# Optimization experiments

Hardware: AMD Instinct MI355X
Metric: run time of the kernel (lower is better)

The kernel has to match this reference:

```python
import jax, jax.numpy as jnp
import numpy as np

WINDOW_SIZE = (8, 8, 8)
DIM = 256
NUM_HEADS = 8
NUM_WINDOWS = 16
BATCH = 128  # num_windows * B
N = int(np.prod(WINDOW_SIZE))  # 512


def _make_rpb_buffers(ws):
    space = len(ws)
    coords = [np.arange(-(w - 1), w, dtype=np.float32) for w in ws]
    rpb = np.stack(np.meshgrid(*coords, indexing='ij'))  # (space, 2w-1, ...)
    for i in range(space):
        rpb[i] = rpb[i] / (ws[i] - 1)
    rpb = np.moveaxis(rpb, 0, -1)[None]  # (1, ..., space)
    rpb = 8.0 * rpb
    rpb = np.sign(rpb) * np.log2(np.abs(rpb) + 1.0) / np.log2(8.0)
    grid = np.stack(np.meshgrid(*[np.arange(w) for w in ws], indexing='ij'))
    g = grid.reshape(space, -1).astype(np.int64)
    dists = g[:, :, None] - g[:, None, :]  # (space, N, N)
    for i in range(space):
        center = max(int(np.prod([2 * w - 1 for w in ws[i + 1:]])), 1)
        dists[i] = (dists[i] + ws[i] - 1) * center
    rpb_idx = dists.sum(0)  # (N, N)
    return rpb.astype(np.float32), rpb_idx.astype(np.int32)


def setup_inputs() -> dict:
    key = jax.random.key(0)
    ks = jax.random.split(key, 8)
    rpb_np, rpb_idx_np = _make_rpb_buffers(WINDOW_SIZE)
    s = 0.02
    return {
        'x': jax.random.normal(ks[0], (BATCH, N, DIM), dtype=jnp.float32),
        'mask': jnp.zeros((NUM_WINDOWS, N, N), dtype=jnp.float32),
        'qkv_w': jax.random.normal(ks[1], (3 * DIM, DIM), dtype=jnp.float32) * s,
        'proj_w': jax.random.normal(ks[2], (DIM, DIM), dtype=jnp.float32) * s,
        'proj_b': jnp.zeros((DIM,), dtype=jnp.float32),
        'cpb_w1': jax.random.normal(ks[3], (512, 3), dtype=jnp.float32) * s,
        'cpb_b1': jnp.zeros((512,), dtype=jnp.float32),
        'cpb_w2': jax.random.normal(ks[4], (NUM_HEADS, 512), dtype=jnp.float32) * s,
        'rpb': jnp.asarray(rpb_np),
        'rpb_idx': jnp.asarray(rpb_idx_np),
    }


def reference(x, mask, qkv_w, proj_w, proj_b, cpb_w1, cpb_b1, cpb_w2, rpb, rpb_idx):
    b, n, c = x.shape
    h = cpb_w2.shape[0]
    hd = c // h
    # qkv projection (no bias), split into q,k,v of shape (b, h, n, hd)
    qkv = jnp.einsum('bnc,oc->bno', x, qkv_w).reshape(b, n, 3, h, hd)
    qkv = jnp.transpose(qkv, (2, 0, 3, 1, 4))
    q, k, v = qkv[0], qkv[1], qkv[2]
    # continuous relative-position bias: MLP over log-spaced coords, gather, sigmoid
    hidden = jax.nn.relu(jnp.einsum('...d,od->...o', rpb, cpb_w1) + cpb_b1)
    table = jnp.einsum('...o,ho->...h', hidden, cpb_w2).reshape(-1, h)  # (prod(2w-1), h)
    rpb_bias = table[rpb_idx.reshape(-1)].reshape(n, n, h)
    rpb_bias = 16.0 * jax.nn.sigmoid(rpb_bias)
    rpb_bias = jnp.transpose(rpb_bias, (2, 0, 1))[None]  # (1, h, n, n)
    # mask (nw, n, n) -> (b, 1, n, n) via repeat along batch
    nw = mask.shape[0]
    m = jnp.tile(mask[:, None, :, :], (b // nw, 1, 1, 1))
    bias = m + rpb_bias  # (b, h, n, n)
    # scaled dot-product attention
    scale = 1.0 / jnp.sqrt(jnp.float32(hd))
    scores = jnp.einsum('bhqd,bhkd->bhqk', q, k) * scale + bias
    attn = jax.nn.softmax(scores, axis=-1)
    out = jnp.einsum('bhqk,bhkd->bhqd', attn, v)
    out = jnp.transpose(out, (0, 2, 1, 3)).reshape(b, n, c)
    out = jnp.einsum('bnc,oc->bno', out, proj_w) + proj_b
    return out
```

## Files before the change

### kernel.cpp

```cpp
#include <hip/hip_runtime.h>
#include <hip/hip_bf16.h>


using u16 = unsigned short;
using u32 = unsigned int;
typedef short bf16x4 __attribute__((ext_vector_type(4)));
typedef short bf16x8 __attribute__((ext_vector_type(8)));
typedef float f32x4 __attribute__((ext_vector_type(4)));

#define QSL 0.25503471f
#define LOG2E 1.44269504f
#define CMB_SHIFT 11.65f

static __device__ __forceinline__ u32 cvt_pk_bf16(float lo, float hi) {
  u32 r;
  asm("v_cvt_pk_bf16_f32 %0, %1, %2" : "=v"(r) : "v"(lo), "v"(hi));
  return r;
}

__global__ __launch_bounds__(512) void cpb_kernel(
    const float* __restrict__ rpb, const float* __restrict__ w1,
    const float* __restrict__ b1, const float* __restrict__ w2,
    float* __restrict__ table16) {
  __shared__ float hid[512];
  const int p = blockIdx.x;
  const int t = threadIdx.x;
  const float r0 = rpb[p * 3 + 0], r1 = rpb[p * 3 + 1], r2 = rpb[p * 3 + 2];
  float hv = fmaf(r0, w1[t * 3 + 0],
             fmaf(r1, w1[t * 3 + 1],
             fmaf(r2, w1[t * 3 + 2], b1[t])));
  hid[t] = fmaxf(hv, 0.0f);
  __syncthreads();
  const int h = t >> 6, lane = t & 63;
  float s = 0.0f;
#pragma unroll
  for (int u = 0; u < 8; ++u)
    s = fmaf(hid[lane + u * 64], w2[h * 512 + lane + u * 64], s);
#pragma unroll
  for (int off = 32; off > 0; off >>= 1) s += __shfl_down(s, off);
  if (lane == 0) table16[p * 8 + h] = 23.08312065f / (1.0f + __expf(-s));
}

__global__ __launch_bounds__(256) void cmb_kernel(
    const int* __restrict__ rpb_idx, const float* __restrict__ table16,
    const float* __restrict__ mask, u16* __restrict__ cmb) {
  const int ij0 = (blockIdx.x * 256 + threadIdx.x) * 4;
  const int w = blockIdx.y;
  const float4 m4 = *reinterpret_cast<const float4*>(mask + (size_t)w * 262144 + ij0);
  const int4 i4 = *reinterpret_cast<const int4*>(rpb_idx + ij0);
  float ta[8], tb[8], tc[8], td[8];
  *reinterpret_cast<float4*>(&ta[0]) = *reinterpret_cast<const float4*>(table16 + i4.x * 8);
  *reinterpret_cast<float4*>(&ta[4]) = *reinterpret_cast<const float4*>(table16 + i4.x * 8 + 4);
  *reinterpret_cast<float4*>(&tb[0]) = *reinterpret_cast<const float4*>(table16 + i4.y * 8);
  *reinterpret_cast<float4*>(&tb[4]) = *reinterpret_cast<const float4*>(table16 + i4.y * 8 + 4);
  *reinterpret_cast<float4*>(&tc[0]) = *reinterpret_cast<const float4*>(table16 + i4.z * 8);
  *reinterpret_cast<float4*>(&tc[4]) = *reinterpret_cast<const float4*>(table16 + i4.z * 8 + 4);
  *reinterpret_cast<float4*>(&td[0]) = *reinterpret_cast<const float4*>(table16 + i4.w * 8);
  *reinterpret_cast<float4*>(&td[4]) = *reinterpret_cast<const float4*>(table16 + i4.w * 8 + 4);
  const float b0 = m4.x * LOG2E - CMB_SHIFT;
  const float b1 = m4.y * LOG2E - CMB_SHIFT;
  const float b2 = m4.z * LOG2E - CMB_SHIFT;
  const float b3 = m4.w * LOG2E - CMB_SHIFT;
  u16* outp = cmb + (size_t)w * 8 * 262144 + ij0;
#pragma unroll
  for (int h = 0; h < 8; ++h) {
    uint2 o;
    o.x = cvt_pk_bf16(ta[h] + b0, tb[h] + b1);
    o.y = cvt_pk_bf16(tc[h] + b2, td[h] + b3);
    *reinterpret_cast<uint2*>(outp + (size_t)h * 262144) = o;
  }
}

__global__ __launch_bounds__(256, 2) void qkv_mfma(
    const float* __restrict__ x, const float* __restrict__ w,
    u16* __restrict__ qbuf, u16* __restrict__ kbuf, u16* __restrict__ vbuf) {
  __shared__ u16 As[128 * 64];
  __shared__ u16 Bs0[128 * 64];
  __shared__ u16 Bs1[128 * 64];
  const int tid = threadIdx.x;
  const int flat = blockIdx.x;
  const int wrk = (flat & 7) * 192 + (flat >> 3);
  const int bm = wrk / 3;
  const int bnp = wrk - bm * 3;
  const int m0 = bm * 128, n0 = bnp * 256;
  const float scl = (bnp == 0) ? QSL : 1.0f;
  u16* dst = bnp == 0 ? qbuf : (bnp == 1 ? kbuf : vbuf);
  const int lane = tid & 63, wid = tid >> 6;
  const int wm = wid >> 1, wn = wid & 1;
  const int lq = lane & 15, g = lane >> 4;
  const f32x4 fz = {0.f, 0.f, 0.f, 0.f};
  f32x4 acc0[4][4], acc1[4][4];
#pragma unroll
  for (int i = 0; i < 4; ++i)
#pragma unroll
    for (int j = 0; j < 4; ++j) { acc0[i][j] = fz; acc1[i][j] = fz; }

  const int r0 = tid >> 3;
  const int ch = tid & 7;
  const int sx = (ch ^ (r0 & 7)) << 3;

  for (int k0 = 0; k0 < 256; k0 += 64) {
    __syncthreads();
#pragma unroll
    for (int rr = 0; rr < 4; ++rr) {
      const int r = r0 + rr * 32;
      const float* ax = x + (size_t)(m0 + r) * 256 + k0 + ch * 8;
      const float4 a0 = *reinterpret_cast<const float4*>(ax);
      const float4 a1 = *reinterpret_cast<const float4*>(ax + 4);
      const float* bx0 = w + (size_t)(n0 + r) * 256 + k0 + ch * 8;
      const float* bx1 = w + (size_t)(n0 + 128 + r) * 256 + k0 + ch * 8;
      const float4 b00 = *reinterpret_cast<const float4*>(bx0);
      const float4 b01 = *reinterpret_cast<const float4*>(bx0 + 4);
      const float4 b10 = *reinterpret_cast<const float4*>(bx1);
      const float4 b11 = *reinterpret_cast<const float4*>(bx1 + 4);
      uint4 pk;
      pk.x = cvt_pk_bf16(a0.x, a0.y); pk.y = cvt_pk_bf16(a0.z, a0.w);
      pk.z = cvt_pk_bf16(a1.x, a1.y); pk.w = cvt_pk_bf16(a1.z, a1.w);
      *reinterpret_cast<uint4*>(&As[r * 64 + sx]) = pk;
      pk.x = cvt_pk_bf16(b00.x * scl, b00.y * scl);
      pk.y = cvt_pk_bf16(b00.z * scl, b00.w * scl);
      pk.z = cvt_pk_bf16(b01.x * scl, b01.y * scl);
      pk.w = cvt_pk_bf16(b01.z * scl, b01.w * scl);
      *reinterpret_cast<uint4*>(&Bs0[r * 64 + sx]) = pk;
      pk.x = cvt_pk_bf16(b10.x * scl, b10.y * scl);
      pk.y = cvt_pk_bf16(b10.z * scl, b10.w * scl);
      pk.z = cvt_pk_bf16(b11.x * scl, b11.y * scl);
      pk.w = cvt_pk_bf16(b11.z * scl, b11.w * scl);
      *reinterpret_cast<uint4*>(&Bs1[r * 64 + sx]) = pk;
    }
    __syncthreads();
#pragma unroll
    for (int ks = 0; ks < 2; ++ks) {
      bf16x8 xf[4];
#pragma unroll
      for (int mt = 0; mt < 4; ++mt) {
        const int row = wm * 64 + mt * 16 + lq;
        xf[mt] = *reinterpret_cast<const bf16x8*>(
            &As[row * 64 + (((ks * 4 + g) ^ (row & 7)) << 3)]);
      }
#pragma unroll
      for (int nt = 0; nt < 4; ++nt) {
        const int row = wn * 64 + nt * 16 + lq;
        const int off = row * 64 + (((ks * 4 + g) ^ (row & 7)) << 3);
        const bf16x8 wf0 = *reinterpret_cast<const bf16x8*>(&Bs0[off]);
        const bf16x8 wf1 = *reinterpret_cast<const bf16x8*>(&Bs1[off]);
#pragma unroll
        for (int mt = 0; mt < 4; ++mt) {
          acc0[mt][nt] = __builtin_amdgcn_mfma_f32_16x16x32_bf16(
              wf0, xf[mt], acc0[mt][nt], 0, 0, 0);
          acc1[mt][nt] = __builtin_amdgcn_mfma_f32_16x16x32_bf16(
              wf1, xf[mt], acc1[mt][nt], 0, 0, 0);
        }
      }
    }
  }
#pragma unroll
  for (int mt = 0; mt < 4; ++mt) {
    const int m = m0 + wm * 64 + mt * 16 + lq;
    const int b = m >> 9, ii = m & 511;
#pragma unroll
    for (int nt = 0; nt < 4; ++nt) {
      const int nn = wn * 64 + nt * 16 + 4 * g;
      {
        const int n = n0 + nn;
        const int h = (n & 255) >> 5;
        const int d = n & 31;
        const size_t off = ((size_t)(b * 8 + h) * 512 + ii) * 32 + d;
        uint2 o2;
        o2.x = cvt_pk_bf16(acc0[mt][nt][0], acc0[mt][nt][1]);
        o2.y = cvt_pk_bf16(acc0[mt][nt][2], acc0[mt][nt][3]);
        *reinterpret_cast<uint2*>(dst + off) = o2;
      }
      {
        const int n = n0 + 128 + nn;
        const int h = (n & 255) >> 5;
        const int d = n & 31;
        const size_t off = ((size_t)(b * 8 + h) * 512 + ii) * 32 + d;
        uint2 o2;
        o2.x = cvt_pk_bf16(acc1[mt][nt][0], acc1[mt][nt][1]);
        o2.y = cvt_pk_bf16(acc1[mt][nt][2], acc1[mt][nt][3]);
        *reinterpret_cast<uint2*>(dst + off) = o2;
      }
    }
  }
}

__global__ __launch_bounds__(256, 2) void attn_mfma(
    u16* qbuf,
    const u16* __restrict__ kbuf, const u16* __restrict__ vbuf,
    const u16* __restrict__ cmb) {
  __shared__ u16 Klds[512 * 32];
  __shared__ u16 Vtlds[32 * 512];
  const int t = threadIdx.x;
  const int qc = blockIdx.x, h = blockIdx.y;
  const int bz = blockIdx.z;
  const int b = ((bz & 15) << 3) | (bz >> 4);
  const size_t bh = (size_t)b * 8 + h;
  const u16* kb = kbuf + bh * 16384;
  const u16* vb = vbuf + bh * 16384;

#pragma unroll
  for (int c = 0; c < 8; ++c) {
    const int cid = t + c * 256;
    const int key = cid >> 2, ch = cid & 3;
    const uint4 kd = *reinterpret_cast<const uint4*>(kb + cid * 8);
    const int idx = key * 32 + ((ch * 8) ^ (((key >> 1) & 3) << 3));
    *reinterpret_cast<uint4*>(&Klds[idx]) = kd;
  }
#pragma unroll
  for (int r = 0; r < 2; ++r) {
    const int n = t + r * 256;
    const uint4 v0 = *reinterpret_cast<const uint4*>(vb + n * 32);
    const uint4 v1 = *reinterpret_cast<const uint4*>(vb + n * 32 + 8);
    const uint4 v2 = *reinterpret_cast<const uint4*>(vb + n * 32 + 16);
    const uint4 v3 = *reinterpret_cast<const uint4*>(vb + n * 32 + 24);
    const u32 wv16[16] = {v0.x, v0.y, v0.z, v0.w, v1.x, v1.y, v1.z, v1.w,
                          v2.x, v2.y, v2.z, v2.w, v3.x, v3.y, v3.z, v3.w};
#pragma unroll
    for (int u = 0; u < 16; ++u) {
      const int d0 = 2 * u, d1 = 2 * u + 1;
      Vtlds[d0 * 512 + (n ^ ((d0 & 7) << 3))] = (u16)(wv16[u] & 0xffffu);
      Vtlds[d1 * 512 + (n ^ ((d1 & 7) << 3))] = (u16)(wv16[u] >> 16);
    }
  }
  __syncthreads();

  const int lane = t & 63;
  const int lq = lane & 15, g = lane >> 4;
  const int wv = t >> 6;
  const int q0 = qc * 256 + wv * 64;

  bf16x8 Qf[4];
  u16* qrowbase = qbuf + bh * 16384;
#pragma unroll
  for (int qt = 0; qt < 4; ++qt)
    Qf[qt] = *reinterpret_cast<const bf16x8*>(qrowbase + (q0 + qt * 16 + lq) * 32 + g * 8);

  const u16* cmbp[4];
  const size_t whbase = (size_t)((b & 15) * 8 + h) * 262144;
#pragma unroll
  for (int qt = 0; qt < 4; ++qt)
    cmbp[qt] = cmb + whbase + (size_t)(q0 + qt * 16 + lq) * 512 + 4 * g;

  const f32x4 fzero = {0.f, 0.f, 0.f, 0.f};
  f32x4 o[2][4];
  f32x4 lsum4[4];
#pragma unroll
  for (int qt = 0; qt < 4; ++qt) {
    lsum4[qt] = fzero;
    o[0][qt] = fzero;
    o[1][qt] = fzero;
  }

  for (int j0 = 0; j0 < 512; j0 += 64) {
    bf16x8 Ak[4];
#pragma unroll
    for (int kt = 0; kt < 4; ++kt) {
      const int key = j0 + kt * 16 + lq;
      const int idx = key * 32 + ((g * 8) ^ (((key >> 1) & 3) << 3));
      Ak[kt] = *reinterpret_cast<const bf16x8*>(&Klds[idx]);
    }
    f32x4 s[4][4];
#pragma unroll
    for (int kt = 0; kt < 4; ++kt)
#pragma unroll
      for (int qt = 0; qt < 4; ++qt) {
        const uint2 cc = *reinterpret_cast<const uint2*>(cmbp[qt] + j0 + kt * 16);
        f32x4 ci;
        ci[0] = __uint_as_float((cc.x & 0xffffu) << 16);
        ci[1] = __uint_as_float(cc.x & 0xffff0000u);
        ci[2] = __uint_as_float((cc.y & 0xffffu) << 16);
        ci[3] = __uint_as_float(cc.y & 0xffff0000u);
        s[kt][qt] = __builtin_amdgcn_mfma_f32_16x16x32_bf16(Ak[kt], Qf[qt], ci, 0, 0, 0);
      }
#pragma unroll
    for (int kt = 0; kt < 4; ++kt) {
      bf16x4 Av[2];
#pragma unroll
      for (int dt = 0; dt < 2; ++dt) {
        const int d = dt * 16 + lq;
        const int n0 = j0 + kt * 16 + 4 * g;
        const int idx = d * 512 + (n0 ^ ((d & 7) << 3));
        Av[dt] = *reinterpret_cast<const bf16x4*>(&Vtlds[idx]);
      }
#pragma unroll
      for (int qt = 0; qt < 4; ++qt) {
        f32x4 p = s[kt][qt];
        p[0] = __builtin_amdgcn_exp2f(p[0]);
        p[1] = __builtin_amdgcn_exp2f(p[1]);
        p[2] = __builtin_amdgcn_exp2f(p[2]);
        p[3] = __builtin_amdgcn_exp2f(p[3]);
        lsum4[qt] += p;
        union { u32 u[2]; bf16x4 v; } bp;
        bp.u[0] = cvt_pk_bf16(p[0], p[1]);
        bp.u[1] = cvt_pk_bf16(p[2], p[3]);
        o[0][qt] = __builtin_amdgcn_mfma_f32_16x16x16bf16_1k(Av[0], bp.v, o[0][qt], 0, 0, 0);
        o[1][qt] = __builtin_amdgcn_mfma_f32_16x16x16bf16_1k(Av[1], bp.v, o[1][qt], 0, 0, 0);
      }
    }
  }
#pragma unroll
  for (int qt = 0; qt < 4; ++qt) {
    float l = (lsum4[qt][0] + lsum4[qt][1]) + (lsum4[qt][2] + lsum4[qt][3]);
    l += __shfl_xor(l, 16);
    l += __shfl_xor(l, 32);
    const float inv = 1.0f / l;
    u16* orow = qrowbase + (q0 + qt * 16 + lq) * 32;
#pragma unroll
    for (int dt = 0; dt < 2; ++dt) {
      uint2 w2;
      w2.x = cvt_pk_bf16(o[dt][qt][0] * inv, o[dt][qt][1] * inv);
      w2.y = cvt_pk_bf16(o[dt][qt][2] * inv, o[dt][qt][3] * inv);
      *reinterpret_cast<uint2*>(orow + dt * 16 + 4 * g) = w2;
    }
  }
}

__global__ __launch_bounds__(256, 2) void proj_mfma(
    const u16* __restrict__ abuf, const float* __restrict__ w,
    const float* __restrict__ pb, float* __restrict__ out) {
  __shared__ u16 As[128 * 64];
  __shared__ u16 Bs0[128 * 64];
  __shared__ u16 Bs1[128 * 64];
  const int tid = threadIdx.x;
  const int bm = blockIdx.x;
  const int m0 = bm * 128;
  const int lane = tid & 63, wid = tid >> 6;
  const int wm = wid >> 1, wn = wid & 1;
  const int lq = lane & 15, g = lane >> 4;
  const f32x4 fz = {0.f, 0.f, 0.f, 0.f};
  f32x4 acc0[4][4], acc1[4][4];
#pragma unroll
  for (int i = 0; i < 4; ++i)
#pragma unroll
    for (int j = 0; j < 4; ++j) { acc0[i][j] = fz; acc1[i][j] = fz; }

  const int r0 = tid >> 3;
  const int ch = tid & 7;
  const int sx = (ch ^ (r0 & 7)) << 3;
  const int ab = m0 >> 9;
  const u16* abase = abuf + (size_t)ab * 8 * 16384;
  const int dA0 = (ch & 3) * 8;

  for (int k0 = 0; k0 < 256; k0 += 64) {
    const int hA0 = (k0 >> 5) + (ch >> 2);
    __syncthreads();
#pragma unroll
    for (int rr = 0; rr < 4; ++rr) {
      const int r = r0 + rr * 32;
      const uint4 ga = *reinterpret_cast<const uint4*>(
          abase + ((size_t)hA0 * 512 + ((m0 & 511) + r)) * 32 + dA0);
      const float* bx0 = w + (size_t)r * 256 + k0 + ch * 8;
      const float* bx1 = w + (size_t)(128 + r) * 256 + k0 + ch * 8;
      const float4 b00 = *reinterpret_cast<const float4*>(bx0);
      const float4 b01 = *reinterpret_cast<const float4*>(bx0 + 4);
      const float4 b10 = *reinterpret_cast<const float4*>(bx1);
      const float4 b11 = *reinterpret_cast<const float4*>(bx1 + 4);
      *reinterpret_cast<uint4*>(&As[r * 64 + sx]) = ga;
      uint4 pk;
      pk.x = cvt_pk_bf16(b00.x, b00.y); pk.y = cvt_pk_bf16(b00.z, b00.w);
      pk.z = cvt_pk_bf16(b01.x, b01.y); pk.w = cvt_pk_bf16(b01.z, b01.w);
      *reinterpret_cast<uint4*>(&Bs0[r * 64 + sx]) = pk;
      pk.x = cvt_pk_bf16(b10.x, b10.y); pk.y = cvt_pk_bf16(b10.z, b10.w);
      pk.z = cvt_pk_bf16(b11.x, b11.y); pk.w = cvt_pk_bf16(b11.z, b11.w);
      *reinterpret_cast<uint4*>(&Bs1[r * 64 + sx]) = pk;
    }
    __syncthreads();
#pragma unroll
    for (int ks = 0; ks < 2; ++ks) {
      bf16x8 xf[4];
#pragma unroll
      for (int mt = 0; mt < 4; ++mt) {
        const int row = wm * 64 + mt * 16 + lq;
        xf[mt] = *reinterpret_cast<const bf16x8*>(
            &As[row * 64 + (((ks * 4 + g) ^ (row & 7)) << 3)]);
      }
#pragma unroll
      for (int nt = 0; nt < 4; ++nt) {
        const int row = wn * 64 + nt * 16 + lq;
        const int off = row * 64 + (((ks * 4 + g) ^ (row & 7)) << 3);
        const bf16x8 wf0 = *reinterpret_cast<const bf16x8*>(&Bs0[off]);
        const bf16x8 wf1 = *reinterpret_cast<const bf16x8*>(&Bs1[off]);
#pragma unroll
        for (int mt = 0; mt < 4; ++mt) {
          acc0[mt][nt] = __builtin_amdgcn_mfma_f32_16x16x32_bf16(
              wf0, xf[mt], acc0[mt][nt], 0, 0, 0);
          acc1[mt][nt] = __builtin_amdgcn_mfma_f32_16x16x32_bf16(
              wf1, xf[mt], acc1[mt][nt], 0, 0, 0);
        }
      }
    }
  }
#pragma unroll
  for (int mt = 0; mt < 4; ++mt) {
    const int m = m0 + wm * 64 + mt * 16 + lq;
#pragma unroll
    for (int nt = 0; nt < 4; ++nt) {
      const int n = wn * 64 + nt * 16 + 4 * g;
      const float4 pb0 = *reinterpret_cast<const float4*>(pb + n);
      *reinterpret_cast<float4*>(out + (size_t)m * 256 + n) =
          make_float4(acc0[mt][nt][0] + pb0.x, acc0[mt][nt][1] + pb0.y,
                      acc0[mt][nt][2] + pb0.z, acc0[mt][nt][3] + pb0.w);
      const float4 pb1 = *reinterpret_cast<const float4*>(pb + 128 + n);
      *reinterpret_cast<float4*>(out + (size_t)m * 256 + 128 + n) =
          make_float4(acc1[mt][nt][0] + pb1.x, acc1[mt][nt][1] + pb1.y,
                      acc1[mt][nt][2] + pb1.z, acc1[mt][nt][3] + pb1.w);
    }
  }
}

extern "C" void kernel_launch(void* const* d_in, const int* in_sizes, int n_in,
                              void* d_out, int out_size, void* d_ws, size_t ws_size,
                              hipStream_t stream) {
  const float* x = (const float*)d_in[0];
  const float* mask = (const float*)d_in[1];
  const float* qkv_w = (const float*)d_in[2];
  const float* proj_w = (const float*)d_in[3];
  const float* proj_b = (const float*)d_in[4];
  const float* cpb_w1 = (const float*)d_in[5];
  const float* cpb_b1 = (const float*)d_in[6];
  const float* cpb_w2 = (const float*)d_in[7];
  const float* rpb = (const float*)d_in[8];
  const int* rpb_idx = (const int*)d_in[9];
  float* out = (float*)d_out;

  char* ws = (char*)d_ws;
  u16* qbuf = (u16*)(ws);
  u16* kbuf = (u16*)(ws + 33554432);
  u16* vbuf = (u16*)(ws + 67108864);
  u16* cmb = (u16*)(ws + 100663296);
  float* table16 = (float*)(ws + 167772160);

  cpb_kernel<<<3375, 512, 0, stream>>>(rpb, cpb_w1, cpb_b1, cpb_w2, table16);
  cmb_kernel<<<dim3(256, 16), 256, 0, stream>>>(rpb_idx, table16, mask, cmb);
  qkv_mfma<<<1536, 256, 0, stream>>>(x, qkv_w, qbuf, kbuf, vbuf);
  attn_mfma<<<dim3(2, 8, 128), 256, 0, stream>>>(qbuf, kbuf, vbuf, cmb);
  proj_mfma<<<512, 256, 0, stream>>>(qbuf, proj_w, proj_b, out);
}
```

Measured before the change: 275.9 us.

## Prefetch next A tile into registers in GEMMs and loop windows in cmb kernel

In the qkv and proj GEMMs, the next k-step's A-operand global loads are issued into registers right after the shared-memory barrier, so their latency overlaps the MFMA work of the current step. The cmb kernel now loops over all 16 windows inside each thread, so the rpb_idx and table gathers are done once per thread instead of once per window. The cost is higher register pressure in the GEMMs, which run at 2 blocks per CU. The cmb grid also shrinks to 256 blocks, which may underfill the GPU for a kernel that is mostly store-bound.

Result: faster. 254.5 us (-7.7%).

```diff
diff --git a/kernel.cpp b/kernel.cpp
--- a/kernel.cpp
+++ b/kernel.cpp
@@ -45,8 +45,6 @@
     const int* __restrict__ rpb_idx, const float* __restrict__ table16,
     const float* __restrict__ mask, u16* __restrict__ cmb) {
   const int ij0 = (blockIdx.x * 256 + threadIdx.x) * 4;
-  const int w = blockIdx.y;
-  const float4 m4 = *reinterpret_cast<const float4*>(mask + (size_t)w * 262144 + ij0);
   const int4 i4 = *reinterpret_cast<const int4*>(rpb_idx + ij0);
   float ta[8], tb[8], tc[8], td[8];
   *reinterpret_cast<float4*>(&ta[0]) = *reinterpret_cast<const float4*>(table16 + i4.x * 8);
@@ -57,17 +55,21 @@
   *reinterpret_cast<float4*>(&tc[4]) = *reinterpret_cast<const float4*>(table16 + i4.z * 8 + 4);
   *reinterpret_cast<float4*>(&td[0]) = *reinterpret_cast<const float4*>(table16 + i4.w * 8);
   *reinterpret_cast<float4*>(&td[4]) = *reinterpret_cast<const float4*>(table16 + i4.w * 8 + 4);
-  const float b0 = m4.x * LOG2E - CMB_SHIFT;
-  const float b1 = m4.y * LOG2E - CMB_SHIFT;
-  const float b2 = m4.z * LOG2E - CMB_SHIFT;
-  const float b3 = m4.w * LOG2E - CMB_SHIFT;
-  u16* outp = cmb + (size_t)w * 8 * 262144 + ij0;
-#pragma unroll
-  for (int h = 0; h < 8; ++h) {
-    uint2 o;
-    o.x = cvt_pk_bf16(ta[h] + b0, tb[h] + b1);
-    o.y = cvt_pk_bf16(tc[h] + b2, td[h] + b3);
-    *reinterpret_cast<uint2*>(outp + (size_t)h * 262144) = o;
+#pragma unroll
+  for (int w = 0; w < 16; ++w) {
+    const float4 m4 = *reinterpret_cast<const float4*>(mask + (size_t)w * 262144 + ij0);
+    const float b0 = m4.x * LOG2E - CMB_SHIFT;
+    const float b1 = m4.y * LOG2E - CMB_SHIFT;
+    const float b2 = m4.z * LOG2E - CMB_SHIFT;
+    const float b3 = m4.w * LOG2E - CMB_SHIFT;
+    u16* outp = cmb + (size_t)w * 8 * 262144 + ij0;
+#pragma unroll
+    for (int h = 0; h < 8; ++h) {
+      uint2 o;
+      o.x = cvt_pk_bf16(ta[h] + b0, tb[h] + b1);
+      o.y = cvt_pk_bf16(tc[h] + b2, td[h] + b3);
+      *reinterpret_cast<uint2*>(outp + (size_t)h * 262144) = o;
+    }
   }
 }
 
@@ -99,14 +101,23 @@
   const int ch = tid & 7;
   const int sx = (ch ^ (r0 & 7)) << 3;
 
-  for (int k0 = 0; k0 < 256; k0 += 64) {
-    __syncthreads();
+  float4 ga[4][2];
+  auto gloadA = [&](int k0) {
 #pragma unroll
     for (int rr = 0; rr < 4; ++rr) {
       const int r = r0 + rr * 32;
       const float* ax = x + (size_t)(m0 + r) * 256 + k0 + ch * 8;
-      const float4 a0 = *reinterpret_cast<const float4*>(ax);
-      const float4 a1 = *reinterpret_cast<const float4*>(ax + 4);
+      ga[rr][0] = *reinterpret_cast<const float4*>(ax);
+      ga[rr][1] = *reinterpret_cast<const float4*>(ax + 4);
+    }
+  };
+
+  gloadA(0);
+  for (int k0 = 0; k0 < 256; k0 += 64) {
+    __syncthreads();
+#pragma unroll
+    for (int rr = 0; rr < 4; ++rr) {
+      const int r = r0 + rr * 32;
       const float* bx0 = w + (size_t)(n0 + r) * 256 + k0 + ch * 8;
       const float* bx1 = w + (size_t)(n0 + 128 + r) * 256 + k0 + ch * 8;
       const float4 b00 = *reinterpret_cast<const float4*>(bx0);
@@ -114,8 +125,10 @@
       const float4 b10 = *reinterpret_cast<const float4*>(bx1);
       const float4 b11 = *reinterpret_cast<const float4*>(bx1 + 4);
       uint4 pk;
-      pk.x = cvt_pk_bf16(a0.x, a0.y); pk.y = cvt_pk_bf16(a0.z, a0.w);
-      pk.z = cvt_pk_bf16(a1.x, a1.y); pk.w = cvt_pk_bf16(a1.z, a1.w);
+      pk.x = cvt_pk_bf16(ga[rr][0].x, ga[rr][0].y);
+      pk.y = cvt_pk_bf16(ga[rr][0].z, ga[rr][0].w);
+      pk.z = cvt_pk_bf16(ga[rr][1].x, ga[rr][1].y);
+      pk.w = cvt_pk_bf16(ga[rr][1].z, ga[rr][1].w);
       *reinterpret_cast<uint4*>(&As[r * 64 + sx]) = pk;
       pk.x = cvt_pk_bf16(b00.x * scl, b00.y * scl);
       pk.y = cvt_pk_bf16(b00.z * scl, b00.w * scl);
@@ -129,6 +142,7 @@
       *reinterpret_cast<uint4*>(&Bs1[r * 64 + sx]) = pk;
     }
     __syncthreads();
+    if (k0 + 64 < 256) gloadA(k0 + 64);
 #pragma unroll
     for (int ks = 0; ks < 2; ++ks) {
       bf16x8 xf[4];
@@ -342,21 +356,30 @@
   const u16* abase = abuf + (size_t)ab * 8 * 16384;
   const int dA0 = (ch & 3) * 8;
 
-  for (int k0 = 0; k0 < 256; k0 += 64) {
+  uint4 gaq[4];
+  auto gloadA = [&](int k0) {
     const int hA0 = (k0 >> 5) + (ch >> 2);
-    __syncthreads();
 #pragma unroll
     for (int rr = 0; rr < 4; ++rr) {
       const int r = r0 + rr * 32;
-      const uint4 ga = *reinterpret_cast<const uint4*>(
+      gaq[rr] = *reinterpret_cast<const uint4*>(
           abase + ((size_t)hA0 * 512 + ((m0 & 511) + r)) * 32 + dA0);
+    }
+  };
+
+  gloadA(0);
+  for (int k0 = 0; k0 < 256; k0 += 64) {
+    __syncthreads();
+#pragma unroll
+    for (int rr = 0; rr < 4; ++rr) {
+      const int r = r0 + rr * 32;
       const float* bx0 = w + (size_t)r * 256 + k0 + ch * 8;
       const float* bx1 = w + (size_t)(128 + r) * 256 + k0 + ch * 8;
       const float4 b00 = *reinterpret_cast<const float4*>(bx0);
       const float4 b01 = *reinterpret_cast<const float4*>(bx0 + 4);
       const float4 b10 = *reinterpret_cast<const float4*>(bx1);
       const float4 b11 = *reinterpret_cast<const float4*>(bx1 + 4);
-      *reinterpret_cast<uint4*>(&As[r * 64 + sx]) = ga;
+      *reinterpret_cast<uint4*>(&As[r * 64 + sx]) = gaq[rr];
       uint4 pk;
       pk.x = cvt_pk_bf16(b00.x, b00.y); pk.y = cvt_pk_bf16(b00.z, b00.w);
       pk.z = cvt_pk_bf16(b01.x, b01.y); pk.w = cvt_pk_bf16(b01.z, b01.w);
@@ -366,6 +389,7 @@
       *reinterpret_cast<uint4*>(&Bs1[r * 64 + sx]) = pk;
     }
     __syncthreads();
+    if (k0 + 64 < 256) gloadA(k0 + 64);
 #pragma unroll
     for (int ks = 0; ks < 2; ++ks) {
       bf16x8 xf[4];
@@ -432,7 +456,7 @@
   float* table16 = (float*)(ws + 167772160);
 
   cpb_kernel<<<3375, 512, 0, stream>>>(rpb, cpb_w1, cpb_b1, cpb_w2, table16);
-  cmb_kernel<<<dim3(256, 16), 256, 0, stream>>>(rpb_idx, table16, mask, cmb);
+  cmb_kernel<<<256, 256, 0, stream>>>(rpb_idx, table16, mask, cmb);
   qkv_mfma<<<1536, 256, 0, stream>>>(x, qkv_w, qbuf, kbuf, vbuf);
   attn_mfma<<<dim3(2, 8, 128), 256, 0, stream>>>(qbuf, kbuf, vbuf, cmb);
   proj_mfma<<<512, 256, 0, stream>>>(qbuf, proj_w, proj_b, out);
```
